# Optimization experiments

Hardware: AMD Instinct MI355X
Metric: run time of the kernel (lower is better)

Reference implementation:

```python
import jax, jax.numpy as jnp
import numpy as np

NBITS = 14   # bits in absolute-position binary encoding
RELCLIP = 32 # relative position clamp -> 65 buckets


def setup_inputs() -> dict:
    key = jax.random.key(0)
    ks = jax.random.split(key, 16)
    L, N = 768, 256
    seq_dim, msa_dim, m_dim, z_dim = 22, 23, 256, 128
    sc = lambda fan_in: 1.0 / np.sqrt(fan_in)
    return {
        "seq": jax.random.normal(ks[0], (L, seq_dim), jnp.float32),
        "msa": jax.random.normal(ks[1], (N, L, msa_dim), jnp.float32),
        "Wmsa": jax.random.normal(ks[2], (msa_dim, m_dim), jnp.float32) * sc(msa_dim),
        "bmsa": jnp.zeros((m_dim,), jnp.float32),
        "Ws": jax.random.normal(ks[3], (seq_dim, m_dim), jnp.float32) * sc(seq_dim),
        "bs": jnp.zeros((m_dim,), jnp.float32),
        "Wq": jax.random.normal(ks[4], (seq_dim, z_dim), jnp.float32) * sc(seq_dim),
        "bq": jnp.zeros((z_dim,), jnp.float32),
        "Wk": jax.random.normal(ks[5], (seq_dim, z_dim), jnp.float32) * sc(seq_dim),
        "bk": jnp.zeros((z_dim,), jnp.float32),
        "Wpos": jax.random.normal(ks[6], (2 * RELCLIP + 1, z_dim), jnp.float32) * sc(65),
        "bpos": jnp.zeros((z_dim,), jnp.float32),
        "Wpos2": jax.random.normal(ks[7], (NBITS, m_dim), jnp.float32) * sc(NBITS),
        "bpos2": jnp.zeros((m_dim,), jnp.float32),
    }


def reference(seq, msa, Wmsa, bmsa, Ws, bs, Wq, bq, Wk, bk, Wpos, bpos, Wpos2, bpos2):
    N, L, _ = msa.shape
    idx = jnp.arange(L)

    # --- MSA branch: msalinear(msa) + slinear(seq) + poslinear2(bits) ---
    s = seq @ Ws + bs                                   # [L, m_dim]
    m = jnp.einsum('nld,dm->nlm', msa, Wmsa) + bmsa     # [N, L, m_dim]
    # absolute-position binary code (L, 14); float one-hot bits @ W2 == linear
    bits = ((idx[:, None] & (1 << jnp.arange(NBITS))) > 0).astype(seq.dtype)
    p = bits @ Wpos2 + bpos2                            # [L, m_dim]
    m = m + s[None, :, :] + p[None, :, :]               # broadcast add

    # --- pair branch: q[j] + k[i] + relpos embedding gather ---
    sq = seq @ Wq + bq                                  # [L, z_dim]
    sk = seq @ Wk + bk                                  # [L, z_dim]
    rel = jnp.clip(idx[None, :] - idx[:, None], -RELCLIP, RELCLIP) + RELCLIP  # [L,L]
    # one_hot(rel, 65) @ Wpos == Wpos[rel] (embedding gather, same math)
    z = sq[None, :, :] + sk[:, None, :] + (Wpos[rel] + bpos)  # [L, L, z_dim]
    return m, z
```

## Files before the change

### kernel.cpp

```cpp
#include <hip/hip_runtime.h>

#define L_SEQ   768
#define N_MSA   256
#define SEQ_D   22
#define MSA_D   23
#define M_DIM   256
#define Z_DIM   128
#define NBITS   14
#define RELCLIP 32
#define ROWS    16

__global__ __launch_bounds__(256) void precompute_kernel(
    const float* __restrict__ seq, const float* __restrict__ Ws,
    const float* __restrict__ bs,  const float* __restrict__ bmsa,
    const float* __restrict__ Wq,  const float* __restrict__ bq,
    const float* __restrict__ Wk,  const float* __restrict__ bk,
    const float* __restrict__ Wpos2, const float* __restrict__ bpos2,
    float* __restrict__ add_m, float* __restrict__ sq_t, float* __restrict__ sk_t) {
  const int l   = blockIdx.x;
  const int tid = threadIdx.x;
  __shared__ float srow[SEQ_D];
  if (tid < SEQ_D) srow[tid] = seq[l * SEQ_D + tid];
  __syncthreads();

  float acc = bs[tid] + bpos2[tid] + bmsa[tid];
#pragma unroll
  for (int d = 0; d < SEQ_D; ++d) acc += srow[d] * Ws[d * M_DIM + tid];
#pragma unroll
  for (int k = 0; k < NBITS; ++k)
    if ((l >> k) & 1) acc += Wpos2[k * M_DIM + tid];
  add_m[l * M_DIM + tid] = acc;

  if (tid < Z_DIM) {
    float aq = bq[tid], ak = bk[tid];
#pragma unroll
    for (int d = 0; d < SEQ_D; ++d) {
      const float sv = srow[d];
      aq += sv * Wq[d * Z_DIM + tid];
      ak += sv * Wk[d * Z_DIM + tid];
    }
    sq_t[l * Z_DIM + tid] = aq;
    sk_t[l * Z_DIM + tid] = ak;
  }
}

__global__ __launch_bounds__(256) void m_kernel(
    const float* __restrict__ msa, const float* __restrict__ Wmsa,
    const float* __restrict__ add_m, float* __restrict__ out_m) {
  const int tid = threadIdx.x;
  float w[MSA_D];
#pragma unroll
  for (int k = 0; k < MSA_D; ++k) w[k] = Wmsa[k * M_DIM + tid];

  const long r0 = (long)blockIdx.x * ROWS;
  const int  l0 = (int)(r0 % L_SEQ);
  const float* __restrict__ mrow = msa + r0 * MSA_D;

#pragma unroll
  for (int r = 0; r < ROWS; ++r) {
    float acc = add_m[(l0 + r) * M_DIM + tid];
#pragma unroll
    for (int k = 0; k < MSA_D; ++k) acc += mrow[r * MSA_D + k] * w[k];
    out_m[(r0 + r) * M_DIM + tid] = acc;
  }
}

__global__ __launch_bounds__(256) void z_kernel(
    const float* __restrict__ sq_t, const float* __restrict__ sk_t,
    const float* __restrict__ Wpos, const float* __restrict__ bpos,
    float* __restrict__ out_z) {
  const int i      = blockIdx.x >> 3;
  const int jchunk = blockIdx.x & 7;
  const int c4     = threadIdx.x & 31;
  const int jlane  = threadIdx.x >> 5;

  const float4* __restrict__ sq4 = (const float4*)sq_t;
  const float4* __restrict__ wp4 = (const float4*)Wpos;

  float4 base = ((const float4*)sk_t)[i * (Z_DIM / 4) + c4];
  const float4 bp = ((const float4*)bpos)[c4];
  base.x += bp.x; base.y += bp.y; base.z += bp.z; base.w += bp.w;

  float4* __restrict__ out4 = (float4*)out_z + (long)i * (L_SEQ * (Z_DIM / 4));
  const int jend = jchunk * 96 + 96;
  for (int j = jchunk * 96 + jlane; j < jend; j += 8) {
    const float4 q = sq4[j * (Z_DIM / 4) + c4];
    int rel = j - i;
    rel = rel < -RELCLIP ? -RELCLIP : (rel > RELCLIP ? RELCLIP : rel);
    rel += RELCLIP;
    const float4 wv = wp4[rel * (Z_DIM / 4) + c4];
    float4 o;
    o.x = base.x + q.x + wv.x;
    o.y = base.y + q.y + wv.y;
    o.z = base.z + q.z + wv.z;
    o.w = base.w + q.w + wv.w;
    out4[(long)j * (Z_DIM / 4) + c4] = o;
  }
}

extern "C" void kernel_launch(void* const* d_in, const int* in_sizes, int n_in,
                              void* d_out, int out_size, void* d_ws, size_t ws_size,
                              hipStream_t stream) {
  const float* seq   = (const float*)d_in[0];
  const float* msa   = (const float*)d_in[1];
  const float* Wmsa  = (const float*)d_in[2];
  const float* bmsa  = (const float*)d_in[3];
  const float* Ws    = (const float*)d_in[4];
  const float* bs    = (const float*)d_in[5];
  const float* Wq    = (const float*)d_in[6];
  const float* bq    = (const float*)d_in[7];
  const float* Wk    = (const float*)d_in[8];
  const float* bk    = (const float*)d_in[9];
  const float* Wpos  = (const float*)d_in[10];
  const float* bpos  = (const float*)d_in[11];
  const float* Wpos2 = (const float*)d_in[12];
  const float* bpos2 = (const float*)d_in[13];

  float* out_m = (float*)d_out;
  float* out_z = out_m + (long)N_MSA * L_SEQ * M_DIM;

  float* add_m = (float*)d_ws;
  float* sq_t  = add_m + L_SEQ * M_DIM;
  float* sk_t  = sq_t + L_SEQ * Z_DIM;

  precompute_kernel<<<L_SEQ, 256, 0, stream>>>(seq, Ws, bs, bmsa, Wq, bq, Wk, bk,
                                               Wpos2, bpos2, add_m, sq_t, sk_t);
  m_kernel<<<(N_MSA * L_SEQ) / ROWS, 256, 0, stream>>>(msa, Wmsa, add_m, out_m);
  z_kernel<<<L_SEQ * 8, 256, 0, stream>>>(sq_t, sk_t, Wpos, bpos, out_z);
}
```

Before: 641.0 us.

## Fuse MSA and pair kernels into one interleaved launch with clamp-region fast paths

New measurement: 607.4 us. 1.06x faster.

```diff
diff --git a/kernel.cpp b/kernel.cpp
--- a/kernel.cpp
+++ b/kernel.cpp
@@ -8,15 +8,19 @@
 #define Z_DIM   128
 #define NBITS   14
 #define RELCLIP 32
-#define ROWS    16
+
+#define M_ROWS_PER_BLOCK 32
+#define MBLOCKS ((N_MSA * L_SEQ) / M_ROWS_PER_BLOCK)
+#define ZBLOCKS (L_SEQ * 8)
 
 __global__ __launch_bounds__(256) void precompute_kernel(
     const float* __restrict__ seq, const float* __restrict__ Ws,
     const float* __restrict__ bs,  const float* __restrict__ bmsa,
     const float* __restrict__ Wq,  const float* __restrict__ bq,
     const float* __restrict__ Wk,  const float* __restrict__ bk,
+    const float* __restrict__ bpos,
     const float* __restrict__ Wpos2, const float* __restrict__ bpos2,
-    float* __restrict__ add_m, float* __restrict__ sq_t, float* __restrict__ sk_t) {
+    float* __restrict__ add_m, float* __restrict__ sq_t, float* __restrict__ skb_t) {
   const int l   = blockIdx.x;
   const int tid = threadIdx.x;
   __shared__ float srow[SEQ_D];
@@ -24,77 +28,104 @@
   __syncthreads();
 
   float acc = bs[tid] + bpos2[tid] + bmsa[tid];
-#pragma unroll
-  for (int d = 0; d < SEQ_D; ++d) acc += srow[d] * Ws[d * M_DIM + tid];
-#pragma unroll
+#pragma unroll 2
+  for (int d = 0; d < SEQ_D; ++d) acc = fmaf(srow[d], Ws[d * M_DIM + tid], acc);
+#pragma unroll 2
   for (int k = 0; k < NBITS; ++k)
     if ((l >> k) & 1) acc += Wpos2[k * M_DIM + tid];
   add_m[l * M_DIM + tid] = acc;
 
   if (tid < Z_DIM) {
-    float aq = bq[tid], ak = bk[tid];
-#pragma unroll
+    float aq = bq[tid], ak = bk[tid] + bpos[tid];
+#pragma unroll 2
     for (int d = 0; d < SEQ_D; ++d) {
       const float sv = srow[d];
-      aq += sv * Wq[d * Z_DIM + tid];
-      ak += sv * Wk[d * Z_DIM + tid];
+      aq = fmaf(sv, Wq[d * Z_DIM + tid], aq);
+      ak = fmaf(sv, Wk[d * Z_DIM + tid], ak);
     }
     sq_t[l * Z_DIM + tid] = aq;
-    sk_t[l * Z_DIM + tid] = ak;
+    skb_t[l * Z_DIM + tid] = ak;
   }
 }
 
-__global__ __launch_bounds__(256) void m_kernel(
+__global__ __launch_bounds__(256) void fused_kernel(
     const float* __restrict__ msa, const float* __restrict__ Wmsa,
-    const float* __restrict__ add_m, float* __restrict__ out_m) {
-  const int tid = threadIdx.x;
-  float w[MSA_D];
+    const float* __restrict__ add_m, const float* __restrict__ sq_t,
+    const float* __restrict__ skb_t, const float* __restrict__ Wpos,
+    float* __restrict__ out_m, float* __restrict__ out_z) {
+  const int bid = blockIdx.x >> 1;
+
+  if (blockIdx.x & 1) {
+    const int tid = threadIdx.x;
+    float w[MSA_D];
 #pragma unroll
-  for (int k = 0; k < MSA_D; ++k) w[k] = Wmsa[k * M_DIM + tid];
+    for (int k = 0; k < MSA_D; ++k) w[k] = Wmsa[k * M_DIM + tid];
 
-  const long r0 = (long)blockIdx.x * ROWS;
-  const int  l0 = (int)(r0 % L_SEQ);
-  const float* __restrict__ mrow = msa + r0 * MSA_D;
+    const long r0 = (long)bid * M_ROWS_PER_BLOCK;
+    const int  l0 = (int)(r0 % L_SEQ);
+    const float* __restrict__ mrow = msa + r0 * MSA_D;
+    const float* __restrict__ arow = add_m + (long)l0 * M_DIM + tid;
+    float* __restrict__ orow = out_m + r0 * M_DIM + tid;
 
+#pragma unroll 2
+    for (int r = 0; r < M_ROWS_PER_BLOCK; ++r) {
+      float acc = arow[r * M_DIM];
 #pragma unroll
-  for (int r = 0; r < ROWS; ++r) {
-    float acc = add_m[(l0 + r) * M_DIM + tid];
-#pragma unroll
-    for (int k = 0; k < MSA_D; ++k) acc += mrow[r * MSA_D + k] * w[k];
-    out_m[(r0 + r) * M_DIM + tid] = acc;
-  }
-}
+      for (int k = 0; k < MSA_D; ++k)
+        acc = fmaf(mrow[r * MSA_D + k], w[k], acc);
+      orow[r * M_DIM] = acc;
+    }
+  } else {
+    const int i  = bid >> 3;
+    const int j0 = (bid & 7) * 96;
+    const int c4 = threadIdx.x & 31;
+    const int jl = threadIdx.x >> 5;
 
-__global__ __launch_bounds__(256) void z_kernel(
-    const float* __restrict__ sq_t, const float* __restrict__ sk_t,
-    const float* __restrict__ Wpos, const float* __restrict__ bpos,
-    float* __restrict__ out_z) {
-  const int i      = blockIdx.x >> 3;
-  const int jchunk = blockIdx.x & 7;
-  const int c4     = threadIdx.x & 31;
-  const int jlane  = threadIdx.x >> 5;
+    const float4* __restrict__ sq4 = (const float4*)sq_t;
+    const float4* __restrict__ wp4 = (const float4*)Wpos;
 
-  const float4* __restrict__ sq4 = (const float4*)sq_t;
-  const float4* __restrict__ wp4 = (const float4*)Wpos;
+    float4 base = ((const float4*)skb_t)[i * (Z_DIM / 4) + c4];
+    float4* __restrict__ out4 =
+        (float4*)out_z + ((long)i * L_SEQ + j0) * (Z_DIM / 4);
 
-  float4 base = ((const float4*)sk_t)[i * (Z_DIM / 4) + c4];
-  const float4 bp = ((const float4*)bpos)[c4];
-  base.x += bp.x; base.y += bp.y; base.z += bp.z; base.w += bp.w;
-
-  float4* __restrict__ out4 = (float4*)out_z + (long)i * (L_SEQ * (Z_DIM / 4));
-  const int jend = jchunk * 96 + 96;
-  for (int j = jchunk * 96 + jlane; j < jend; j += 8) {
-    const float4 q = sq4[j * (Z_DIM / 4) + c4];
-    int rel = j - i;
-    rel = rel < -RELCLIP ? -RELCLIP : (rel > RELCLIP ? RELCLIP : rel);
-    rel += RELCLIP;
-    const float4 wv = wp4[rel * (Z_DIM / 4) + c4];
-    float4 o;
-    o.x = base.x + q.x + wv.x;
-    o.y = base.y + q.y + wv.y;
-    o.z = base.z + q.z + wv.z;
-    o.w = base.w + q.w + wv.w;
-    out4[(long)j * (Z_DIM / 4) + c4] = o;
+    if (j0 - i >= RELCLIP) {
+      const float4 wv = wp4[(2 * RELCLIP) * (Z_DIM / 4) + c4];
+      base.x += wv.x; base.y += wv.y; base.z += wv.z; base.w += wv.w;
+#pragma unroll 2
+      for (int t = 0; t < 12; ++t) {
+        const int j = jl + 8 * t;
+        const float4 q = sq4[(j0 + j) * (Z_DIM / 4) + c4];
+        float4 o;
+        o.x = base.x + q.x; o.y = base.y + q.y;
+        o.z = base.z + q.z; o.w = base.w + q.w;
+        out4[j * (Z_DIM / 4) + c4] = o;
+      }
+    } else if (j0 + 95 - i <= -RELCLIP) {
+      const float4 wv = wp4[c4];
+      base.x += wv.x; base.y += wv.y; base.z += wv.z; base.w += wv.w;
+#pragma unroll 2
+      for (int t = 0; t < 12; ++t) {
+        const int j = jl + 8 * t;
+        const float4 q = sq4[(j0 + j) * (Z_DIM / 4) + c4];
+        float4 o;
+        o.x = base.x + q.x; o.y = base.y + q.y;
+        o.z = base.z + q.z; o.w = base.w + q.w;
+        out4[j * (Z_DIM / 4) + c4] = o;
+      }
+    } else {
+#pragma unroll 2
+      for (int t = 0; t < 12; ++t) {
+        const int j = jl + 8 * t;
+        int rel = (j0 + j) - i;
+        rel = rel < -RELCLIP ? -RELCLIP : (rel > RELCLIP ? RELCLIP : rel);
+        const float4 q  = sq4[(j0 + j) * (Z_DIM / 4) + c4];
+        const float4 wv = wp4[(rel + RELCLIP) * (Z_DIM / 4) + c4];
+        float4 o;
+        o.x = base.x + q.x + wv.x; o.y = base.y + q.y + wv.y;
+        o.z = base.z + q.z + wv.z; o.w = base.w + q.w + wv.w;
+        out4[j * (Z_DIM / 4) + c4] = o;
+      }
+    }
   }
 }
 
@@ -121,10 +152,11 @@
 
   float* add_m = (float*)d_ws;
   float* sq_t  = add_m + L_SEQ * M_DIM;
-  float* sk_t  = sq_t + L_SEQ * Z_DIM;
+  float* skb_t = sq_t + L_SEQ * Z_DIM;
 
   precompute_kernel<<<L_SEQ, 256, 0, stream>>>(seq, Ws, bs, bmsa, Wq, bq, Wk, bk,
-                                               Wpos2, bpos2, add_m, sq_t, sk_t);
-  m_kernel<<<(N_MSA * L_SEQ) / ROWS, 256, 0, stream>>>(msa, Wmsa, add_m, out_m);
-  z_kernel<<<L_SEQ * 8, 256, 0, stream>>>(sq_t, sk_t, Wpos, bpos, out_z);
+                                               bpos, Wpos2, bpos2,
+                                               add_m, sq_t, skb_t);
+  fused_kernel<<<MBLOCKS + ZBLOCKS, 256, 0, stream>>>(msa, Wmsa, add_m, sq_t,
+                                                      skb_t, Wpos, out_m, out_z);
 }
```
